# Kernel optimization log

Hardware: AMD Instinct MI355X
Metric: run time of the kernel (lower is better)

Reference implementation:

```python
import jax, jax.numpy as jnp
from jax import lax
import numpy as np

K = 31      # avg_pool2d kernel_size
PAD = 15    # avg_pool2d padding
EPS = 1.0
GAMMA = 5.0


def _box_avg(x):
    # Separable 31x31 box filter, stride 1, zero padding 15,
    # count_include_pad=True (PyTorch default) -> always divide by K*K.
    s = lax.reduce_window(x, 0.0, lax.add, (1, 1, K, 1), (1, 1, 1, 1),
                          [(0, 0), (0, 0), (PAD, PAD), (0, 0)])
    s = lax.reduce_window(s, 0.0, lax.add, (1, 1, 1, K), (1, 1, 1, 1),
                          [(0, 0), (0, 0), (0, 0), (PAD, PAD)])
    return s / (K * K)


def setup_inputs() -> dict:
    key = jax.random.key(0)
    k1, k2 = jax.random.split(key)
    shape = (64, 1, 512, 512)  # [B, C, H, W]
    inp = jax.random.uniform(k1, shape, dtype=jnp.float32)
    tgt = jax.random.uniform(k2, shape, dtype=jnp.float32)
    return {"input": inp, "target": tgt}


def reference(input, target):
    weight = 1.0 + GAMMA * jnp.abs(_box_avg(target) - target)
    intersection = jnp.sum(input * target * weight)
    denom = jnp.sum(input * weight) + jnp.sum(target * weight)
    dice = (2.0 * intersection + EPS) / (denom + EPS)
    return 1.0 - dice
```

## Files before the change

kernel.cpp:

```cpp
#include <hip/hip_runtime.h>
#include <hip/hip_bf16.h>


#define BATCH 64
#define H     512
#define W     512
#define RBAND 32
#define RING  63
#define NBLK  (BATCH * (H / RBAND))

static __device__ __forceinline__ unsigned pack2(float e, float o) {
    __hip_bfloat162 h = __float22bfloat162_rn(make_float2(e, o));
    unsigned u; __builtin_memcpy(&u, &h, 4); return u;
}
static __device__ __forceinline__ float2 unpk(unsigned u) {
    return make_float2(__uint_as_float(u << 16),
                       __uint_as_float(u & 0xffff0000u));
}

__global__ __launch_bounds__(256, 2) void fused_kernel(const float* __restrict__ tgt,
                                                       const float* __restrict__ inp,
                                                       float4* __restrict__ partials) {
    const int tid  = threadIdx.x;
    const int lane = tid & 63;
    const int wv   = tid >> 6;
    const int g    = blockIdx.x;
    const int blk  = ((g & 7) << 7) | (g >> 3);
    const int band = blk & 15;
    const int b    = blk >> 4;
    const int R0   = band * RBAND;
    const float* timg = tgt + (size_t)b * H * W;
    const float* iimg = inp + (size_t)b * H * W;

    __shared__ __align__(16) unsigned ring[RING * 256];

    const int col0 = lane * 8;
    const int ofs  = lane * 4;

    #pragma unroll
    for (int k = 0; k < 16; ++k) {
        const int idx = 4 * k + wv;
        if (idx < RING) {
            const int row = R0 - 15 + idx;
            float4 v0 = make_float4(0.f, 0.f, 0.f, 0.f), v1 = v0;
            if (row >= 0 && row < H) {
                v0 = *(const float4*)(timg + (size_t)row * W + col0);
                v1 = *(const float4*)(timg + (size_t)row * W + col0 + 4);
            }
            uint4 u;
            u.x = pack2(v0.x, v0.y); u.y = pack2(v0.z, v0.w);
            u.z = pack2(v1.x, v1.y); u.w = pack2(v1.z, v1.w);
            *(uint4*)&ring[idx * 256 + ofs] = u;
        }
    }
    __syncthreads();

    const float mL1 = (lane >= 1) ? 1.f : 0.f;
    const float mR1 = (lane <= 62) ? 1.f : 0.f;
    const float mL2 = (lane >= 2) ? 1.f : 0.f;
    const float mR2 = (lane <= 61) ? 1.f : 0.f;

    const int base = 8 * wv;
    float vr[8];
    #pragma unroll
    for (int k = 0; k < 8; ++k) vr[k] = 0.f;
    #pragma unroll
    for (int jj = 0; jj < 31; ++jj) {
        const uint4 c = *(const uint4*)&ring[(base + jj) * 256 + ofs];
        const float2 e0 = unpk(c.x), e1 = unpk(c.y), e2 = unpk(c.z), e3 = unpk(c.w);
        vr[0] += e0.x; vr[1] += e0.y; vr[2] += e1.x; vr[3] += e1.y;
        vr[4] += e2.x; vr[5] += e2.y; vr[6] += e3.x; vr[7] += e3.y;
    }

    const float inv = 1.0f / 961.0f;
    float aI = 0.f, aA = 0.f, aB = 0.f;

    #pragma unroll
    for (int st = 0; st < 8; ++st) {
        const int h  = R0 + 8 * wv + st;
        const int sl = base + st;

        const float4 i0 = *(const float4*)(iimg + (size_t)h * W + col0);
        const float4 i1 = *(const float4*)(iimg + (size_t)h * W + col0 + 4);
        const uint4  tc = *(const uint4*)&ring[(sl + 15) * 256 + ofs];
        uint4 ua = make_uint4(0u, 0u, 0u, 0u), us = ua;
        if (st < 7) {
            ua = *(const uint4*)&ring[(sl + 31) * 256 + ofs];
            us = *(const uint4*)&ring[sl * 256 + ofs];
        }

        const float p1 = vr[0];
        const float p2 = p1 + vr[1];
        const float p3 = p2 + vr[2];
        const float p4 = p3 + vr[3];
        const float p5 = p4 + vr[4];
        const float p6 = p5 + vr[5];
        const float p7 = p6 + vr[6];
        const float s  = p7 + vr[7];
        const float f1 = s - p1, f2 = s - p2, f3 = s - p3, f4 = s - p4;
        const float f5 = s - p5, f6 = s - p6, f7 = s - p7;

        const float sL1 = __shfl_up(s, 1, 64);
        const float sR1 = __shfl_down(s, 1, 64);
        const float g1 = __shfl_up(f1, 2, 64);
        const float g2 = __shfl_up(f2, 2, 64);
        const float g3 = __shfl_up(f3, 2, 64);
        const float g4 = __shfl_up(f4, 2, 64);
        const float g5 = __shfl_up(f5, 2, 64);
        const float g6 = __shfl_up(f6, 2, 64);
        const float g7 = __shfl_up(f7, 2, 64);
        const float q1 = __shfl_down(p1, 2, 64);
        const float q2 = __shfl_down(p2, 2, 64);
        const float q3 = __shfl_down(p3, 2, 64);
        const float q4 = __shfl_down(p4, 2, 64);
        const float q5 = __shfl_down(p5, 2, 64);
        const float q6 = __shfl_down(p6, 2, 64);
        const float q7 = __shfl_down(p7, 2, 64);

        const float S3 = fmaf(mL1, sL1, fmaf(mR1, sR1, s));
        float win[8];
        win[0] = fmaf(mL2, g1, S3);
        win[1] = fmaf(mL2, g2, fmaf(mR2, q1, S3));
        win[2] = fmaf(mL2, g3, fmaf(mR2, q2, S3));
        win[3] = fmaf(mL2, g4, fmaf(mR2, q3, S3));
        win[4] = fmaf(mL2, g5, fmaf(mR2, q4, S3));
        win[5] = fmaf(mL2, g6, fmaf(mR2, q5, S3));
        win[6] = fmaf(mL2, g7, fmaf(mR2, q6, S3));
        win[7] = fmaf(mR2, q7, S3);

        const float2 t0 = unpk(tc.x), t1 = unpk(tc.y), t2 = unpk(tc.z), t3 = unpk(tc.w);
        const float tv[8] = {t0.x, t0.y, t1.x, t1.y, t2.x, t2.y, t3.x, t3.y};
        const float iv[8] = {i0.x, i0.y, i0.z, i0.w, i1.x, i1.y, i1.z, i1.w};

        #pragma unroll
        for (int k = 0; k < 8; ++k) {
            const float wgt = fmaf(5.0f, fabsf(fmaf(win[k], inv, -tv[k])), 1.0f);
            aI += iv[k] * tv[k] * wgt;
            aA += iv[k] * wgt;
            aB += tv[k] * wgt;
        }

        if (st < 7) {
            const float2 a0 = unpk(ua.x), a1 = unpk(ua.y),
                         a2 = unpk(ua.z), a3 = unpk(ua.w);
            const float2 s0 = unpk(us.x), s1 = unpk(us.y),
                         s2 = unpk(us.z), s3 = unpk(us.w);
            vr[0] += a0.x - s0.x; vr[1] += a0.y - s0.y;
            vr[2] += a1.x - s1.x; vr[3] += a1.y - s1.y;
            vr[4] += a2.x - s2.x; vr[5] += a2.y - s2.y;
            vr[6] += a3.x - s3.x; vr[7] += a3.y - s3.y;
        }
    }

    #pragma unroll
    for (int off = 32; off > 0; off >>= 1) {
        aI += __shfl_down(aI, off, 64);
        aA += __shfl_down(aA, off, 64);
        aB += __shfl_down(aB, off, 64);
    }
    __syncthreads();
    float* rf = (float*)ring;
    if (lane == 0) { rf[wv] = aI; rf[8 + wv] = aA; rf[16 + wv] = aB; }
    __syncthreads();
    if (tid == 0) {
        float4 o;
        o.x = rf[0] + rf[1] + rf[2] + rf[3];
        o.y = rf[8] + rf[9] + rf[10] + rf[11];
        o.z = rf[16] + rf[17] + rf[18] + rf[19];
        o.w = 0.f;
        partials[g] = o;
    }
}

__global__ __launch_bounds__(1024) void reduce_kernel(const float4* __restrict__ partials,
                                                      float* __restrict__ out) {
    const int tid = threadIdx.x;
    const float4 v = partials[tid];
    float aI = v.x, aA = v.y, aB = v.z;
    #pragma unroll
    for (int off = 32; off > 0; off >>= 1) {
        aI += __shfl_down(aI, off, 64);
        aA += __shfl_down(aA, off, 64);
        aB += __shfl_down(aB, off, 64);
    }
    __shared__ float s[3][16];
    const int wvx = tid >> 6, ln = tid & 63;
    if (ln == 0) { s[0][wvx] = aI; s[1][wvx] = aA; s[2][wvx] = aB; }
    __syncthreads();
    if (tid == 0) {
        float I = 0.f, A = 0.f, Bv = 0.f;
        #pragma unroll
        for (int k = 0; k < 16; ++k) { I += s[0][k]; A += s[1][k]; Bv += s[2][k]; }
        out[0] = 1.0f - (2.0f * I + 1.0f) / (A + Bv + 1.0f);
    }
}

extern "C" void kernel_launch(void* const* d_in, const int* in_sizes, int n_in,
                              void* d_out, int out_size, void* d_ws, size_t ws_size,
                              hipStream_t stream) {
    const float* inp = (const float*)d_in[0];
    const float* tgt = (const float*)d_in[1];
    float* out = (float*)d_out;

    float4* partials = (float4*)d_ws;

    fused_kernel<<<NBLK, 256, 0, stream>>>(tgt, inp, partials);
    reduce_kernel<<<1, 1024, 0, stream>>>(partials, out);
}
```

Baseline: 153.7 us.

## Swap filter order: horizontal box sums first, store fp16 row sums in LDS

The horizontal 31-wide box sum now runs once per loaded target row during staging, and the result goes to LDS as fp16. The vertical sliding sum then runs over the stored row sums, which takes the shuffle-heavy horizontal pass out of the per-output loop. Exact fp32 target values are reloaded from global memory for the weight term instead of the bf16 copy. The changes add fp16 rounding of row sums up to 31, extra global target reads, and reduced unrolling.

```diff
diff --git a/kernel.cpp b/kernel.cpp
--- a/kernel.cpp
+++ b/kernel.cpp
@@ -1,22 +1,14 @@
 #include <hip/hip_runtime.h>
-#include <hip/hip_bf16.h>
 
 
 #define BATCH 64
 #define H     512
 #define W     512
 #define RBAND 32
-#define RING  63
+#define SLOTS 62
 #define NBLK  (BATCH * (H / RBAND))
 
-static __device__ __forceinline__ unsigned pack2(float e, float o) {
-    __hip_bfloat162 h = __float22bfloat162_rn(make_float2(e, o));
-    unsigned u; __builtin_memcpy(&u, &h, 4); return u;
-}
-static __device__ __forceinline__ float2 unpk(unsigned u) {
-    return make_float2(__uint_as_float(u << 16),
-                       __uint_as_float(u & 0xffff0000u));
-}
+typedef _Float16 half8 __attribute__((ext_vector_type(8)));
 
 __global__ __launch_bounds__(256, 2) void fused_kernel(const float* __restrict__ tgt,
                                                        const float* __restrict__ inp,
@@ -32,44 +24,82 @@
     const float* timg = tgt + (size_t)b * H * W;
     const float* iimg = inp + (size_t)b * H * W;
 
-    __shared__ __align__(16) unsigned ring[RING * 256];
+    __shared__ __align__(16) unsigned ring[SLOTS * 256];
 
     const int col0 = lane * 8;
     const int ofs  = lane * 4;
-
-    #pragma unroll
-    for (int k = 0; k < 16; ++k) {
-        const int idx = 4 * k + wv;
-        if (idx < RING) {
-            const int row = R0 - 15 + idx;
-            float4 v0 = make_float4(0.f, 0.f, 0.f, 0.f), v1 = v0;
-            if (row >= 0 && row < H) {
-                v0 = *(const float4*)(timg + (size_t)row * W + col0);
-                v1 = *(const float4*)(timg + (size_t)row * W + col0 + 4);
-            }
-            uint4 u;
-            u.x = pack2(v0.x, v0.y); u.y = pack2(v0.z, v0.w);
-            u.z = pack2(v1.x, v1.y); u.w = pack2(v1.z, v1.w);
-            *(uint4*)&ring[idx * 256 + ofs] = u;
-        }
-    }
-    __syncthreads();
 
     const float mL1 = (lane >= 1) ? 1.f : 0.f;
     const float mR1 = (lane <= 62) ? 1.f : 0.f;
     const float mL2 = (lane >= 2) ? 1.f : 0.f;
     const float mR2 = (lane <= 61) ? 1.f : 0.f;
 
+    #pragma unroll 2
+    for (int k = 0; k < 16; ++k) {
+        const int idx = 4 * k + wv;
+        if (idx < SLOTS) {
+            const int row = R0 - 15 + idx;
+            float t[8];
+            #pragma unroll
+            for (int q = 0; q < 8; ++q) t[q] = 0.f;
+            if (row >= 0 && row < H) {
+                const float4 v0 = *(const float4*)(timg + (size_t)row * W + col0);
+                const float4 v1 = *(const float4*)(timg + (size_t)row * W + col0 + 4);
+                t[0] = v0.x; t[1] = v0.y; t[2] = v0.z; t[3] = v0.w;
+                t[4] = v1.x; t[5] = v1.y; t[6] = v1.z; t[7] = v1.w;
+            }
+            const float p1 = t[0];
+            const float p2 = p1 + t[1];
+            const float p3 = p2 + t[2];
+            const float p4 = p3 + t[3];
+            const float p5 = p4 + t[4];
+            const float p6 = p5 + t[5];
+            const float p7 = p6 + t[6];
+            const float s  = p7 + t[7];
+            const float f1 = s - p1, f2 = s - p2, f3 = s - p3, f4 = s - p4;
+            const float f5 = s - p5, f6 = s - p6, f7 = s - p7;
+
+            const float sL1 = __shfl_up(s, 1, 64);
+            const float sR1 = __shfl_down(s, 1, 64);
+            const float g1 = __shfl_up(f1, 2, 64);
+            const float g2 = __shfl_up(f2, 2, 64);
+            const float g3 = __shfl_up(f3, 2, 64);
+            const float g4 = __shfl_up(f4, 2, 64);
+            const float g5 = __shfl_up(f5, 2, 64);
+            const float g6 = __shfl_up(f6, 2, 64);
+            const float g7 = __shfl_up(f7, 2, 64);
+            const float q1 = __shfl_down(p1, 2, 64);
+            const float q2 = __shfl_down(p2, 2, 64);
+            const float q3 = __shfl_down(p3, 2, 64);
+            const float q4 = __shfl_down(p4, 2, 64);
+            const float q5 = __shfl_down(p5, 2, 64);
+            const float q6 = __shfl_down(p6, 2, 64);
+            const float q7 = __shfl_down(p7, 2, 64);
+
+            const float S3 = fmaf(mL1, sL1, fmaf(mR1, sR1, s));
+            half8 hv;
+            hv[0] = (_Float16)fmaf(mL2, g1, S3);
+            hv[1] = (_Float16)fmaf(mL2, g2, fmaf(mR2, q1, S3));
+            hv[2] = (_Float16)fmaf(mL2, g3, fmaf(mR2, q2, S3));
+            hv[3] = (_Float16)fmaf(mL2, g4, fmaf(mR2, q3, S3));
+            hv[4] = (_Float16)fmaf(mL2, g5, fmaf(mR2, q4, S3));
+            hv[5] = (_Float16)fmaf(mL2, g6, fmaf(mR2, q5, S3));
+            hv[6] = (_Float16)fmaf(mL2, g7, fmaf(mR2, q6, S3));
+            hv[7] = (_Float16)fmaf(mR2, q7, S3);
+            *(half8*)&ring[idx * 256 + ofs] = hv;
+        }
+    }
+    __syncthreads();
+
     const int base = 8 * wv;
-    float vr[8];
+    float box[8];
     #pragma unroll
-    for (int k = 0; k < 8; ++k) vr[k] = 0.f;
-    #pragma unroll
+    for (int q = 0; q < 8; ++q) box[q] = 0.f;
+    #pragma unroll 4
     for (int jj = 0; jj < 31; ++jj) {
-        const uint4 c = *(const uint4*)&ring[(base + jj) * 256 + ofs];
-        const float2 e0 = unpk(c.x), e1 = unpk(c.y), e2 = unpk(c.z), e3 = unpk(c.w);
-        vr[0] += e0.x; vr[1] += e0.y; vr[2] += e1.x; vr[3] += e1.y;
-        vr[4] += e2.x; vr[5] += e2.y; vr[6] += e3.x; vr[7] += e3.y;
+        const half8 c = *(const half8*)&ring[(base + jj) * 256 + ofs];
+        #pragma unroll
+        for (int q = 0; q < 8; ++q) box[q] += (float)c[q];
     }
 
     const float inv = 1.0f / 961.0f;
@@ -77,78 +107,29 @@
 
     #pragma unroll
     for (int st = 0; st < 8; ++st) {
-        const int h  = R0 + 8 * wv + st;
-        const int sl = base + st;
+        const int h = R0 + base + st;
+
+        if (st > 0) {
+            const half8 a = *(const half8*)&ring[(base + st + 30) * 256 + ofs];
+            const half8 s = *(const half8*)&ring[(base + st - 1) * 256 + ofs];
+            #pragma unroll
+            for (int q = 0; q < 8; ++q) box[q] += (float)a[q] - (float)s[q];
+        }
 
         const float4 i0 = *(const float4*)(iimg + (size_t)h * W + col0);
         const float4 i1 = *(const float4*)(iimg + (size_t)h * W + col0 + 4);
-        const uint4  tc = *(const uint4*)&ring[(sl + 15) * 256 + ofs];
-        uint4 ua = make_uint4(0u, 0u, 0u, 0u), us = ua;
-        if (st < 7) {
-            ua = *(const uint4*)&ring[(sl + 31) * 256 + ofs];
-            us = *(const uint4*)&ring[sl * 256 + ofs];
-        }
-
-        const float p1 = vr[0];
-        const float p2 = p1 + vr[1];
-        const float p3 = p2 + vr[2];
-        const float p4 = p3 + vr[3];
-        const float p5 = p4 + vr[4];
-        const float p6 = p5 + vr[5];
-        const float p7 = p6 + vr[6];
-        const float s  = p7 + vr[7];
-        const float f1 = s - p1, f2 = s - p2, f3 = s - p3, f4 = s - p4;
-        const float f5 = s - p5, f6 = s - p6, f7 = s - p7;
-
-        const float sL1 = __shfl_up(s, 1, 64);
-        const float sR1 = __shfl_down(s, 1, 64);
-        const float g1 = __shfl_up(f1, 2, 64);
-        const float g2 = __shfl_up(f2, 2, 64);
-        const float g3 = __shfl_up(f3, 2, 64);
-        const float g4 = __shfl_up(f4, 2, 64);
-        const float g5 = __shfl_up(f5, 2, 64);
-        const float g6 = __shfl_up(f6, 2, 64);
-        const float g7 = __shfl_up(f7, 2, 64);
-        const float q1 = __shfl_down(p1, 2, 64);
-        const float q2 = __shfl_down(p2, 2, 64);
-        const float q3 = __shfl_down(p3, 2, 64);
-        const float q4 = __shfl_down(p4, 2, 64);
-        const float q5 = __shfl_down(p5, 2, 64);
-        const float q6 = __shfl_down(p6, 2, 64);
-        const float q7 = __shfl_down(p7, 2, 64);
-
-        const float S3 = fmaf(mL1, sL1, fmaf(mR1, sR1, s));
-        float win[8];
-        win[0] = fmaf(mL2, g1, S3);
-        win[1] = fmaf(mL2, g2, fmaf(mR2, q1, S3));
-        win[2] = fmaf(mL2, g3, fmaf(mR2, q2, S3));
-        win[3] = fmaf(mL2, g4, fmaf(mR2, q3, S3));
-        win[4] = fmaf(mL2, g5, fmaf(mR2, q4, S3));
-        win[5] = fmaf(mL2, g6, fmaf(mR2, q5, S3));
-        win[6] = fmaf(mL2, g7, fmaf(mR2, q6, S3));
-        win[7] = fmaf(mR2, q7, S3);
-
-        const float2 t0 = unpk(tc.x), t1 = unpk(tc.y), t2 = unpk(tc.z), t3 = unpk(tc.w);
-        const float tv[8] = {t0.x, t0.y, t1.x, t1.y, t2.x, t2.y, t3.x, t3.y};
+        const float4 t0 = *(const float4*)(timg + (size_t)h * W + col0);
+        const float4 t1 = *(const float4*)(timg + (size_t)h * W + col0 + 4);
+        const float tv[8] = {t0.x, t0.y, t0.z, t0.w, t1.x, t1.y, t1.z, t1.w};
         const float iv[8] = {i0.x, i0.y, i0.z, i0.w, i1.x, i1.y, i1.z, i1.w};
 
         #pragma unroll
         for (int k = 0; k < 8; ++k) {
-            const float wgt = fmaf(5.0f, fabsf(fmaf(win[k], inv, -tv[k])), 1.0f);
-            aI += iv[k] * tv[k] * wgt;
-            aA += iv[k] * wgt;
-            aB += tv[k] * wgt;
-        }
-
-        if (st < 7) {
-            const float2 a0 = unpk(ua.x), a1 = unpk(ua.y),
-                         a2 = unpk(ua.z), a3 = unpk(ua.w);
-            const float2 s0 = unpk(us.x), s1 = unpk(us.y),
-                         s2 = unpk(us.z), s3 = unpk(us.w);
-            vr[0] += a0.x - s0.x; vr[1] += a0.y - s0.y;
-            vr[2] += a1.x - s1.x; vr[3] += a1.y - s1.y;
-            vr[4] += a2.x - s2.x; vr[5] += a2.y - s2.y;
-            vr[6] += a3.x - s3.x; vr[7] += a3.y - s3.y;
+            const float wgt = fmaf(5.0f, fabsf(fmaf(box[k], inv, -tv[k])), 1.0f);
+            const float tw  = tv[k] * wgt;
+            aI = fmaf(iv[k], tw, aI);
+            aA = fmaf(iv[k], wgt, aA);
+            aB += tw;
         }
     }
 
```

Result: slower. 163.3 us (+6.2%).
